# Kernel tuning notes

Hardware: AMD Instinct MI355X
Metric: run time of the kernel (lower is better)

The kernel has to match this reference:

```python
import jax, jax.numpy as jnp
import numpy as np

EMBED_DIM = 1024
NUM_HEADS = 16
HEAD_DIM = EMBED_DIM // NUM_HEADS


def setup_inputs() -> dict:
    key = jax.random.key(0)
    ks = jax.random.split(key, 9)
    B, S, D = 4, 2048, EMBED_DIM
    s = 1.0 / np.sqrt(D)
    return {
        "x": jax.random.normal(ks[0], (B, S, D), dtype=jnp.float32),
        "Wq": jax.random.normal(ks[1], (D, D), dtype=jnp.float32) * s,
        "bq": jnp.zeros((D,), dtype=jnp.float32),
        "Wk": jax.random.normal(ks[2], (D, D), dtype=jnp.float32) * s,
        "bk": jnp.zeros((D,), dtype=jnp.float32),
        "Wv": jax.random.normal(ks[3], (D, D), dtype=jnp.float32) * s,
        "bv": jnp.zeros((D,), dtype=jnp.float32),
        "Wo": jax.random.normal(ks[4], (D, D), dtype=jnp.float32) * s,
        "bo": jnp.zeros((D,), dtype=jnp.float32),
    }


def reference(x, Wq, bq, Wk, bk, Wv, bv, Wo, bo):
    B, S, D = x.shape
    H, Hd = NUM_HEADS, HEAD_DIM

    def proj(W, b):
        # [B,S,D] -> [B,H,S,Hd]
        y = jnp.einsum('bsd,de->bse', x, W) + b
        return y.reshape(B, S, H, Hd).transpose(0, 2, 1, 3)

    q = proj(Wq, bq)
    k = proj(Wk, bk)
    v = proj(Wv, bv)

    scale = 1.0 / jnp.sqrt(jnp.asarray(Hd, dtype=x.dtype))
    scores = jnp.einsum('bhqd,bhkd->bhqk', q, k) * scale  # [B,H,S,S]
    attn = jax.nn.softmax(scores, axis=-1)
    # dropout is identity in eval/inference mode
    heads = jnp.einsum('bhqk,bhkd->bhqd', attn, v)  # [B,H,S,Hd]
    heads = heads.transpose(0, 2, 1, 3).reshape(B, S, D)
    z = jnp.einsum('bsd,de->bse', heads, Wo) + bo
    return z
```

## Files before the change

kernel.cpp:

```cpp
#include <hip/hip_runtime.h>


typedef __attribute__((ext_vector_type(8))) short bf16x8;
typedef __attribute__((ext_vector_type(4))) float f32x4;

#define MFMA16 __builtin_amdgcn_mfma_f32_16x16x32_bf16

__device__ __forceinline__ unsigned short f2bf(float f) {
  unsigned int u = __float_as_uint(f);
  u += 0x7fff + ((u >> 16) & 1);
  return (unsigned short)(u >> 16);
}

__device__ __forceinline__ void gl2l16(const unsigned short* g, unsigned short* l) {
  __builtin_amdgcn_global_load_lds((const __attribute__((address_space(1))) void*)g,
                                   (__attribute__((address_space(3))) void*)l, 16, 0, 0);
}

__global__ __launch_bounds__(256) void k_prep(const float* __restrict__ x,
                                              unsigned short* __restrict__ xb,
                                              const float* w0, const float* w1,
                                              const float* w2, const float* w3,
                                              unsigned short* o0, unsigned short* o1,
                                              unsigned short* o2, unsigned short* o3) {
  const int bid = blockIdx.x, tid = threadIdx.x;
  if (bid < 8192) {
    int i = (bid * 256 + tid) * 4;
    float4 v = *(const float4*)(x + i);
    ushort4 u;
    u.x = f2bf(v.x); u.y = f2bf(v.y); u.z = f2bf(v.z); u.w = f2bf(v.w);
    *(ushort4*)(xb + i) = u;
  } else {
    __shared__ float t[32][33];
    int tt = bid - 8192;
    int z = tt >> 10, rem = tt & 1023;
    const float* W = z == 0 ? w0 : z == 1 ? w1 : z == 2 ? w2 : w3;
    unsigned short* O = z == 0 ? o0 : z == 1 ? o1 : z == 2 ? o2 : o3;
    int e0 = (rem & 31) * 32, d0 = (rem >> 5) * 32;
    int tx = tid & 31, ty = tid >> 5;
    #pragma unroll
    for (int i = 0; i < 4; i++)
      t[ty + i * 8][tx] = W[(d0 + ty + i * 8) * 1024 + e0 + tx];
    __syncthreads();
    #pragma unroll
    for (int i = 0; i < 4; i++)
      O[(e0 + ty + i * 8) * 1024 + d0 + tx] = f2bf(t[tx][ty + i * 8]);
  }
}

__device__ __forceinline__ void kloop64(const unsigned short* __restrict__ gA,
                                        const unsigned short* __restrict__ gB,
                                        unsigned short* As, unsigned short* Bs,
                                        int w, int fm, int quad, int wr, int wc,
                                        f32x4 (&acc)[4][4]) {
  const int fsw = fm & 7;
  const int cs0 = (quad ^ fsw) * 8;
  const int cs1 = ((quad + 4) ^ fsw) * 8;
  unsigned short* lA = As + w * 2048;
  unsigned short* lB = Bs + w * 2048;

  for (int kb = 0; kb < 1024; kb += 64) {
    __syncthreads();
    #pragma unroll
    for (int i = 0; i < 4; i++) {
      gl2l16(gA + kb + i * 8192, lA + i * 512);
      gl2l16(gB + kb + i * 8192, lB + i * 512);
    }
    __syncthreads();
    #pragma unroll
    for (int kh = 0; kh < 2; kh++) {
      const int cs = kh ? cs1 : cs0;
      bf16x8 af[4], bfr[4];
      #pragma unroll
      for (int mt = 0; mt < 4; mt++)
        af[mt] = *(const bf16x8*)&As[(wr + mt * 16 + fm) * 64 + cs];
      #pragma unroll
      for (int nt = 0; nt < 4; nt++)
        bfr[nt] = *(const bf16x8*)&Bs[(wc + nt * 16 + fm) * 64 + cs];
      #pragma unroll
      for (int mt = 0; mt < 4; mt++)
        #pragma unroll
        for (int nt = 0; nt < 4; nt++)
          acc[mt][nt] = MFMA16(af[mt], bfr[nt], acc[mt][nt], 0, 0, 0);
    }
  }
}

__global__ __launch_bounds__(256) void gemm_qkv(const unsigned short* __restrict__ A,
                                                const unsigned short* __restrict__ BtQ,
                                                const unsigned short* __restrict__ BtK,
                                                const unsigned short* __restrict__ BtV,
                                                const float* __restrict__ biq,
                                                const float* __restrict__ bik,
                                                const float* __restrict__ biv,
                                                unsigned short* __restrict__ oq,
                                                unsigned short* __restrict__ ok,
                                                unsigned short* __restrict__ ov,
                                                float qscale) {
  const int z = blockIdx.z;
  const unsigned short* Bt = z == 0 ? BtQ : z == 1 ? BtK : BtV;
  const float* bias = z == 0 ? biq : z == 1 ? bik : biv;
  unsigned short* out = z == 0 ? oq : z == 1 ? ok : ov;
  const float scale = z == 0 ? qscale : 1.0f;

  const int tid = threadIdx.x;
  const int lane = tid & 63, w = tid >> 6;
  const int wr = (w >> 1) * 64, wc = (w & 1) * 64;
  const int fm = lane & 15, quad = lane >> 4;
  const int bm0 = blockIdx.y * 128, bn0 = blockIdx.x * 128;

  __shared__ unsigned short As[128 * 64];
  __shared__ unsigned short Bs[128 * 64];

  f32x4 acc[4][4] = {};

  const int srow = lane >> 3;
  const int sswz = ((lane & 7) ^ srow) * 8;
  const unsigned short* gA = A + (size_t)(bm0 + w * 32 + srow) * 1024 + sswz;
  const unsigned short* gB = Bt + (size_t)(bn0 + w * 32 + srow) * 1024 + sswz;

  kloop64(gA, gB, As, Bs, w, fm, quad, wr, wc, acc);

  float bv[4];
  #pragma unroll
  for (int nt = 0; nt < 4; nt++) bv[nt] = bias[bn0 + wc + nt * 16 + fm];

  #pragma unroll
  for (int mt = 0; mt < 4; mt++) {
    #pragma unroll
    for (int nt = 0; nt < 4; nt++) {
      #pragma unroll
      for (int r = 0; r < 4; r++) {
        int row = bm0 + wr + mt * 16 + quad * 4 + r;
        int col = bn0 + wc + nt * 16 + fm;
        float v = (acc[mt][nt][r] + bv[nt]) * scale;
        int b = row >> 11, s = row & 2047, h = col >> 6, hd = col & 63;
        if (z < 2)
          out[(((b << 4) + h) * 2048 + s) * 64 + hd] = f2bf(v);
        else
          out[(((b << 4) + h) * 64 + hd) * 2048 + s] = f2bf(v);
      }
    }
  }
}

__global__ __launch_bounds__(256) void gemm_out(const unsigned short* __restrict__ A,
                                                const unsigned short* __restrict__ Bt,
                                                const float* __restrict__ bias,
                                                float* __restrict__ out) {
  const int tid = threadIdx.x;
  const int lane = tid & 63, w = tid >> 6;
  const int wr = (w >> 1) * 64, wc = (w & 1) * 64;
  const int fm = lane & 15, quad = lane >> 4;
  const int bm0 = blockIdx.y * 128, bn0 = blockIdx.x * 128;

  __shared__ unsigned short As[128 * 64];
  __shared__ unsigned short Bs[128 * 64];

  f32x4 acc[4][4] = {};

  const int srow = lane >> 3;
  const int sswz = ((lane & 7) ^ srow) * 8;
  const unsigned short* gA = A + (size_t)(bm0 + w * 32 + srow) * 1024 + sswz;
  const unsigned short* gB = Bt + (size_t)(bn0 + w * 32 + srow) * 1024 + sswz;

  kloop64(gA, gB, As, Bs, w, fm, quad, wr, wc, acc);

  float bv[4];
  #pragma unroll
  for (int nt = 0; nt < 4; nt++) bv[nt] = bias[bn0 + wc + nt * 16 + fm];

  #pragma unroll
  for (int mt = 0; mt < 4; mt++)
    #pragma unroll
    for (int nt = 0; nt < 4; nt++)
      #pragma unroll
      for (int r = 0; r < 4; r++) {
        int row = bm0 + wr + mt * 16 + quad * 4 + r;
        int col = bn0 + wc + nt * 16 + fm;
        out[(size_t)row * 1024 + col] = acc[mt][nt][r] + bv[nt];
      }
}

__global__ __launch_bounds__(256) void k_attn(const unsigned short* __restrict__ q,
                                              const unsigned short* __restrict__ k,
                                              const unsigned short* __restrict__ vt,
                                              unsigned short* __restrict__ heads) {
  const int tid = threadIdx.x, lane = tid & 63, w = tid >> 6;
  const int fm = lane & 15, quad = lane >> 4, k0 = quad * 8;
  const int bh = blockIdx.x, qt = blockIdx.y;
  const int b = bh >> 4, h = bh & 15;
  const unsigned short* qg = q + (size_t)bh * 2048 * 64;
  const unsigned short* kg = k + (size_t)bh * 2048 * 64;
  const unsigned short* vg = vt + (size_t)bh * 64 * 2048;

  __shared__ unsigned short Ks[64 * 64];
  __shared__ unsigned short Vs[64 * 64];
  __shared__ unsigned short Ps[4][16 * 68];

  const int sr = lane >> 3;
  const int sswz = ((lane & 7) ^ sr) * 8;
  const unsigned short* gK = kg + (w * 16 + sr) * 64 + sswz;
  const unsigned short* gV = vg + (size_t)(w * 16 + sr) * 2048 + sswz;
  unsigned short* lK = Ks + w * 1024;
  unsigned short* lV = Vs + w * 1024;

  bf16x8 aq[2][2];
  #pragma unroll
  for (int mt = 0; mt < 2; mt++)
    #pragma unroll
    for (int kh = 0; kh < 2; kh++)
      aq[mt][kh] = *(const bf16x8*)&qg[(qt * 128 + w * 32 + mt * 16 + fm) * 64 + kh * 32 + k0];

  bf16x8 onesf;
  #pragma unroll
  for (int i = 0; i < 8; i++) onesf[i] = (short)0x3F80;

  f32x4 o[2][4] = {};
  f32x4 la[2] = {};
  const f32x4 zf = {0.f, 0.f, 0.f, 0.f};
  const int fsw = fm & 7;

  for (int kb = 0; kb < 32; kb++) {
    __syncthreads();
    gl2l16(gK + kb * 4096, lK);
    gl2l16(gK + kb * 4096 + 512, lK + 512);
    gl2l16(gV + kb * 64, lV);
    gl2l16(gV + kb * 64 + 8 * 2048, lV + 512);
    __syncthreads();

    f32x4 s[2][4];
    #pragma unroll
    for (int nt = 0; nt < 4; nt++) {
      bf16x8 bK0 = *(const bf16x8*)&Ks[(nt * 16 + fm) * 64 + ((quad ^ fsw) * 8)];
      s[0][nt] = MFMA16(aq[0][0], bK0, zf, 0, 0, 0);
      s[1][nt] = MFMA16(aq[1][0], bK0, zf, 0, 0, 0);
      bf16x8 bK1 = *(const bf16x8*)&Ks[(nt * 16 + fm) * 64 + (((4 + quad) ^ fsw) * 8)];
      s[0][nt] = MFMA16(aq[0][1], bK1, s[0][nt], 0, 0, 0);
      s[1][nt] = MFMA16(aq[1][1], bK1, s[1][nt], 0, 0, 0);
    }

    bf16x8 ap[2][2];
    #pragma unroll
    for (int mt = 0; mt < 2; mt++) {
      #pragma unroll
      for (int nt = 0; nt < 4; nt++)
        #pragma unroll
        for (int r = 0; r < 4; r++) {
          float p = __builtin_amdgcn_exp2f(s[mt][nt][r]);
          unsigned int t = __float_as_uint(p) + 0x8000u;
          Ps[w][(quad * 4 + r) * 68 + nt * 16 + fm] = (unsigned short)(t >> 16);
        }
      ap[mt][0] = *(const bf16x8*)&Ps[w][fm * 68 + k0];
      ap[mt][1] = *(const bf16x8*)&Ps[w][fm * 68 + 32 + k0];
    }

    #pragma unroll
    for (int ks = 0; ks < 2; ks++) {
      la[0] = MFMA16(ap[0][ks], onesf, la[0], 0, 0, 0);
      la[1] = MFMA16(ap[1][ks], onesf, la[1], 0, 0, 0);
      #pragma unroll
      for (int nt = 0; nt < 4; nt++) {
        bf16x8 bV = *(const bf16x8*)&Vs[(nt * 16 + fm) * 64 + (((ks * 4 + quad) ^ fsw) * 8)];
        o[0][nt] = MFMA16(ap[0][ks], bV, o[0][nt], 0, 0, 0);
        o[1][nt] = MFMA16(ap[1][ks], bV, o[1][nt], 0, 0, 0);
      }
    }
  }

  #pragma unroll
  for (int mt = 0; mt < 2; mt++)
    #pragma unroll
    for (int r = 0; r < 4; r++) {
      float inv = 1.0f / la[mt][r];
      int srw = qt * 128 + w * 32 + mt * 16 + quad * 4 + r;
      #pragma unroll
      for (int nt = 0; nt < 4; nt++)
        heads[(size_t)(b * 2048 + srw) * 1024 + h * 64 + nt * 16 + fm] =
            f2bf(o[mt][nt][r] * inv);
    }
}

extern "C" void kernel_launch(void* const* d_in, const int* in_sizes, int n_in,
                              void* d_out, int out_size, void* d_ws, size_t ws_size,
                              hipStream_t stream) {
  const float* x  = (const float*)d_in[0];
  const float* Wq = (const float*)d_in[1];
  const float* bq = (const float*)d_in[2];
  const float* Wk = (const float*)d_in[3];
  const float* bk = (const float*)d_in[4];
  const float* Wv = (const float*)d_in[5];
  const float* bv = (const float*)d_in[6];
  const float* Wo = (const float*)d_in[7];
  const float* bo = (const float*)d_in[8];
  float* out = (float*)d_out;

  char* ws = (char*)d_ws;
  unsigned short* xb  = (unsigned short*)(ws);
  unsigned short* wtq = (unsigned short*)(ws + (16u << 20));
  unsigned short* wtk = (unsigned short*)(ws + (18u << 20));
  unsigned short* wtv = (unsigned short*)(ws + (20u << 20));
  unsigned short* wto = (unsigned short*)(ws + (22u << 20));
  unsigned short* qb  = (unsigned short*)(ws + (24u << 20));
  unsigned short* kb2 = (unsigned short*)(ws + (40u << 20));
  unsigned short* vtb = (unsigned short*)(ws + (56u << 20));
  unsigned short* hb  = (unsigned short*)(ws + (72u << 20));

  k_prep<<<12288, 256, 0, stream>>>(x, xb, Wq, Wk, Wv, Wo, wtq, wtk, wtv, wto);

  const float qscale = 0.125f * 1.44269504088896f;
  gemm_qkv<<<dim3(8, 64, 3), 256, 0, stream>>>(xb, wtq, wtk, wtv, bq, bk, bv,
                                               qb, kb2, vtb, qscale);

  k_attn<<<dim3(64, 16), 256, 0, stream>>>(qb, kb2, vtb, hb);

  gemm_out<<<dim3(8, 64), 256, 0, stream>>>(hb, wto, bo, out);
}
```

Before: 304.5 us.

## Keep softmax probabilities in registers by transposing QK MFMA operands

Swaps the operands of the QK^T MFMA so each lane holds score values along the key dimension. The exponentiated probabilities can then be packed into bf16 pairs and fed straight to the PV MFMA as the A operand, with no round trip through LDS. The V loads are rearranged into two 4-element reads to match the new k-index ordering of P. It also adds an occupancy hint of 4 blocks per SM to launch_bounds. This removes the per-iteration LDS writes and reads of P, at the cost of more register pressure and split V loads.

Measured after the change: 292.0 us. 4.1% less time.

```diff
diff --git a/kernel.cpp b/kernel.cpp
--- a/kernel.cpp
+++ b/kernel.cpp
@@ -2,7 +2,9 @@
 
 
 typedef __attribute__((ext_vector_type(8))) short bf16x8;
+typedef __attribute__((ext_vector_type(4))) short bf16x4;
 typedef __attribute__((ext_vector_type(4))) float f32x4;
+typedef __attribute__((ext_vector_type(4))) unsigned int u32x4;
 
 #define MFMA16 __builtin_amdgcn_mfma_f32_16x16x32_bf16
 
@@ -10,6 +12,19 @@
   unsigned int u = __float_as_uint(f);
   u += 0x7fff + ((u >> 16) & 1);
   return (unsigned short)(u >> 16);
+}
+
+__device__ __forceinline__ unsigned int pkbf(float lo, float hi) {
+  unsigned int a = __float_as_uint(lo) + 0x8000u;
+  unsigned int b = __float_as_uint(hi) + 0x8000u;
+  return __builtin_amdgcn_perm(b, a, 0x07060302u);
+}
+
+__device__ __forceinline__ bf16x8 pack4(unsigned int a, unsigned int b,
+                                        unsigned int c, unsigned int d) {
+  union { u32x4 u; bf16x8 v; } t;
+  t.u = (u32x4){a, b, c, d};
+  return t.v;
 }
 
 __device__ __forceinline__ void gl2l16(const unsigned short* g, unsigned short* l) {
@@ -182,10 +197,10 @@
       }
 }
 
-__global__ __launch_bounds__(256) void k_attn(const unsigned short* __restrict__ q,
-                                              const unsigned short* __restrict__ k,
-                                              const unsigned short* __restrict__ vt,
-                                              unsigned short* __restrict__ heads) {
+__global__ __launch_bounds__(256, 4) void k_attn(const unsigned short* __restrict__ q,
+                                                 const unsigned short* __restrict__ k,
+                                                 const unsigned short* __restrict__ vt,
+                                                 unsigned short* __restrict__ heads) {
   const int tid = threadIdx.x, lane = tid & 63, w = tid >> 6;
   const int fm = lane & 15, quad = lane >> 4, k0 = quad * 8;
   const int bh = blockIdx.x, qt = blockIdx.y;
@@ -196,7 +211,6 @@
 
   __shared__ unsigned short Ks[64 * 64];
   __shared__ unsigned short Vs[64 * 64];
-  __shared__ unsigned short Ps[4][16 * 68];
 
   const int sr = lane >> 3;
   const int sswz = ((lane & 7) ^ sr) * 8;
@@ -220,6 +234,7 @@
   f32x4 la[2] = {};
   const f32x4 zf = {0.f, 0.f, 0.f, 0.f};
   const int fsw = fm & 7;
+  const int vq4 = (quad & 1) * 4;
 
   for (int kb = 0; kb < 32; kb++) {
     __syncthreads();
@@ -229,41 +244,41 @@
     gl2l16(gV + kb * 64 + 8 * 2048, lV + 512);
     __syncthreads();
 
-    f32x4 s[2][4];
+    unsigned int pw[2][8];
     #pragma unroll
     for (int nt = 0; nt < 4; nt++) {
       bf16x8 bK0 = *(const bf16x8*)&Ks[(nt * 16 + fm) * 64 + ((quad ^ fsw) * 8)];
-      s[0][nt] = MFMA16(aq[0][0], bK0, zf, 0, 0, 0);
-      s[1][nt] = MFMA16(aq[1][0], bK0, zf, 0, 0, 0);
+      f32x4 s0 = MFMA16(bK0, aq[0][0], zf, 0, 0, 0);
+      f32x4 s1 = MFMA16(bK0, aq[1][0], zf, 0, 0, 0);
       bf16x8 bK1 = *(const bf16x8*)&Ks[(nt * 16 + fm) * 64 + (((4 + quad) ^ fsw) * 8)];
-      s[0][nt] = MFMA16(aq[0][1], bK1, s[0][nt], 0, 0, 0);
-      s[1][nt] = MFMA16(aq[1][1], bK1, s[1][nt], 0, 0, 0);
-    }
-
-    bf16x8 ap[2][2];
-    #pragma unroll
-    for (int mt = 0; mt < 2; mt++) {
-      #pragma unroll
-      for (int nt = 0; nt < 4; nt++)
-        #pragma unroll
-        for (int r = 0; r < 4; r++) {
-          float p = __builtin_amdgcn_exp2f(s[mt][nt][r]);
-          unsigned int t = __float_as_uint(p) + 0x8000u;
-          Ps[w][(quad * 4 + r) * 68 + nt * 16 + fm] = (unsigned short)(t >> 16);
-        }
-      ap[mt][0] = *(const bf16x8*)&Ps[w][fm * 68 + k0];
-      ap[mt][1] = *(const bf16x8*)&Ps[w][fm * 68 + 32 + k0];
-    }
+      s0 = MFMA16(bK1, aq[0][1], s0, 0, 0, 0);
+      s1 = MFMA16(bK1, aq[1][1], s1, 0, 0, 0);
+      pw[0][nt * 2 + 0] = pkbf(__builtin_amdgcn_exp2f(s0[0]), __builtin_amdgcn_exp2f(s0[1]));
+      pw[0][nt * 2 + 1] = pkbf(__builtin_amdgcn_exp2f(s0[2]), __builtin_amdgcn_exp2f(s0[3]));
+      pw[1][nt * 2 + 0] = pkbf(__builtin_amdgcn_exp2f(s1[0]), __builtin_amdgcn_exp2f(s1[1]));
+      pw[1][nt * 2 + 1] = pkbf(__builtin_amdgcn_exp2f(s1[2]), __builtin_amdgcn_exp2f(s1[3]));
+    }
+
+    bf16x8 ap0k0 = pack4(pw[0][0], pw[0][1], pw[0][2], pw[0][3]);
+    bf16x8 ap0k1 = pack4(pw[0][4], pw[0][5], pw[0][6], pw[0][7]);
+    bf16x8 ap1k0 = pack4(pw[1][0], pw[1][1], pw[1][2], pw[1][3]);
+    bf16x8 ap1k1 = pack4(pw[1][4], pw[1][5], pw[1][6], pw[1][7]);
 
     #pragma unroll
     for (int ks = 0; ks < 2; ks++) {
-      la[0] = MFMA16(ap[0][ks], onesf, la[0], 0, 0, 0);
-      la[1] = MFMA16(ap[1][ks], onesf, la[1], 0, 0, 0);
-      #pragma unroll
-      for (int nt = 0; nt < 4; nt++) {
-        bf16x8 bV = *(const bf16x8*)&Vs[(nt * 16 + fm) * 64 + (((ks * 4 + quad) ^ fsw) * 8)];
-        o[0][nt] = MFMA16(ap[0][ks], bV, o[0][nt], 0, 0, 0);
-        o[1][nt] = MFMA16(ap[1][ks], bV, o[1][nt], 0, 0, 0);
+      bf16x8 a0 = ks ? ap0k1 : ap0k0;
+      bf16x8 a1 = ks ? ap1k1 : ap1k0;
+      la[0] = MFMA16(a0, onesf, la[0], 0, 0, 0);
+      la[1] = MFMA16(a1, onesf, la[1], 0, 0, 0);
+      #pragma unroll
+      for (int ntO = 0; ntO < 4; ntO++) {
+        const int row = (ntO * 16 + fm) * 64;
+        const int g1 = ks * 4 + (quad >> 1);
+        bf16x4 v0 = *(const bf16x4*)&Vs[row + ((g1 ^ fsw) * 8) + vq4];
+        bf16x4 v1 = *(const bf16x4*)&Vs[row + (((g1 + 2) ^ fsw) * 8) + vq4];
+        bf16x8 bV = __builtin_shufflevector(v0, v1, 0, 1, 2, 3, 4, 5, 6, 7);
+        o[0][ntO] = MFMA16(a0, bV, o[0][ntO], 0, 0, 0);
+        o[1][ntO] = MFMA16(a1, bV, o[1][ntO], 0, 0, 0);
       }
     }
   }
```
